# Performance work log

Measured on AMD Instinct MI355X. Metric: run time of the kernel, lower is better.

Reference implementation:

```python
import jax, jax.numpy as jnp
import numpy as np

EPS = 1e-8


def setup_inputs() -> dict:
    key = jax.random.key(0)
    k1, k2, k3 = jax.random.split(key, 3)
    B, N, M, C = 4, 4096, 16384, 256
    xyz = jax.random.normal(k1, (B * N, 3), dtype=jnp.float32)
    new_xyz = jax.random.normal(k2, (B * M, 3), dtype=jnp.float32)
    feat = jax.random.normal(k3, (B * N, C), dtype=jnp.float32)
    offset = jnp.arange(1, B + 1, dtype=jnp.int64) * N      # [4096, 8192, 12288, 16384]
    new_offset = jnp.arange(1, B + 1, dtype=jnp.int64) * M  # [16384, ..., 65536]
    return {"xyz": xyz, "new_xyz": new_xyz, "feat": feat,
            "offset": offset, "new_offset": new_offset, "k": 3}


def _interpolate(xyz_b, new_xyz_b, feat_b, k):
    # xyz_b: [B,N,3], new_xyz_b: [B,M,3], feat_b: [B,N,C]
    # pairwise squared distances via GEMM: [B,M,N]
    q2 = jnp.sum(new_xyz_b * new_xyz_b, axis=-1, keepdims=True)        # [B,M,1]
    s2 = jnp.sum(xyz_b * xyz_b, axis=-1)[:, None, :]                   # [B,1,N]
    cross = jnp.einsum('bmd,bnd->bmn', new_xyz_b, xyz_b)               # [B,M,N]
    d2 = q2 + s2 - 2.0 * cross                                         # [B,M,N]
    neg_d2, idx = jax.lax.top_k(-d2, k)                                # [B,M,k]
    dist = jnp.sqrt(jnp.maximum(-neg_d2, 1e-12))                       # euclidean, like knnquery
    dist_recip = 1.0 / (dist + EPS)
    weight = dist_recip / jnp.sum(dist_recip, axis=-1, keepdims=True)  # [B,M,k]
    gathered = jax.vmap(lambda f, i: f[i])(feat_b, idx)                # [B,M,k,C]
    return jnp.einsum('bmkc,bmk->bmc', gathered, weight)               # [B,M,C]


def reference(xyz, new_xyz, feat, offset, new_offset, k):
    B = offset.shape[0]
    N = xyz.shape[0] // B
    M = new_xyz.shape[0] // B
    C = feat.shape[1]
    # uniform offsets -> reshape into per-cloud batches
    out = _interpolate(xyz.reshape(B, N, 3), new_xyz.reshape(B, M, 3),
                       feat.reshape(B, N, C), k)
    return out.reshape(B * M, C)
```

## Files before the change

kernel.cpp:

```cpp
#include <hip/hip_runtime.h>
#include <float.h>


#define QPL   2
#define QPB   128
#define SPLIT 8
#define KEY_INIT 0x7FEFFFFFFFFFFFFFULL

typedef float v2f __attribute__((ext_vector_type(2)));

__global__ void pack_pts(const float* __restrict__ xyz,
                         float4* __restrict__ pts, int total) {
    int i = blockIdx.x * blockDim.x + threadIdx.x;
    if (i < total) {
        const float sx = xyz[(size_t)i * 3 + 0];
        const float sy = xyz[(size_t)i * 3 + 1];
        const float sz = xyz[(size_t)i * 3 + 2];
        const float s2 = __fadd_rn(__fadd_rn(__fmul_rn(sx, sx), __fmul_rn(sy, sy)),
                                   __fmul_rn(sz, sz));
        pts[i] = make_float4(sx, sy, sz, s2);
    }
}

__device__ __forceinline__ double mk_key(float d2, int j) {
    unsigned long long u =
        ((unsigned long long)(unsigned)__float_as_uint(d2) << 32) | (unsigned)j;
    return __longlong_as_double(u);
}

__device__ __forceinline__ v2f dist2_pair(const v2f qx2, const v2f qy2,
                                          const v2f qz2, const v2f q22,
                                          const float4 p) {
    #pragma clang fp contract(off)
    const v2f px = {p.x, p.x};
    const v2f py = {p.y, p.y};
    const v2f pz = {p.z, p.z};
    const v2f pw = {p.w, p.w};
    const v2f t0 = qx2 * px;
    const v2f t1 = qy2 * py;
    const v2f t2 = t0 + t1;
    const v2f t3 = qz2 * pz;
    const v2f cr = t2 + t3;
    const v2f qs = q22 + pw;
    const v2f cc = cr + cr;
    const v2f d2 = qs - cc;
    return d2;
}

__device__ __forceinline__ float dist2_scalar(float qx, float qy, float qz,
                                              float q2, const float4 p) {
    #pragma clang fp contract(off)
    const float t0 = qx * p.x;
    const float t1 = qy * p.y;
    const float t2 = t0 + t1;
    const float t3 = qz * p.z;
    const float cr = t2 + t3;
    const float qs = q2 + p.w;
    const float cc = cr + cr;
    const float d2 = qs - cc;
    return d2;
}

template <int CHUNK>
__global__ __launch_bounds__(512, 4) void fp_knn_main(
    const float* __restrict__ new_xyz,
    const float4* __restrict__ pts,
    const float4* __restrict__ feat4,
    float4* __restrict__ out4,
    int N, int blocks_per_batch)
{
    __shared__ double s_k[SPLIT][QPB][3];
    __shared__ float  s_w[QPB][3];
    __shared__ int    s_j[QPB][3];

    int g = blockIdx.x;
    if (gridDim.x == 512 && blocks_per_batch == 128) {
        const int xcd = g & 7, slot = g >> 3;
        g = (xcd >> 1) * 128 + (xcd & 1) * 64 + slot;
    }

    const int tid  = threadIdx.x;
    const int lane = tid & 63;
    const int b    = g / blocks_per_batch;
    const int src_base = b * N;
    const int m0 = g * QPB + lane;
    const int m1 = m0 + 64;

    const float q0x = new_xyz[(size_t)m0 * 3 + 0];
    const float q0y = new_xyz[(size_t)m0 * 3 + 1];
    const float q0z = new_xyz[(size_t)m0 * 3 + 2];
    const float q1x = new_xyz[(size_t)m1 * 3 + 0];
    const float q1y = new_xyz[(size_t)m1 * 3 + 1];
    const float q1z = new_xyz[(size_t)m1 * 3 + 2];
    const float q02 = __fadd_rn(__fadd_rn(__fmul_rn(q0x, q0x), __fmul_rn(q0y, q0y)),
                                __fmul_rn(q0z, q0z));
    const float q12 = __fadd_rn(__fadd_rn(__fmul_rn(q1x, q1x), __fmul_rn(q1y, q1y)),
                                __fmul_rn(q1z, q1z));
    const v2f qx2 = {q0x, q1x};
    const v2f qy2 = {q0y, q1y};
    const v2f qz2 = {q0z, q1z};
    const v2f q22 = {q02, q12};

    const int cw    = tid >> 6;
    const int cbase = cw * CHUNK;
    const float4* __restrict__ cp = pts + src_base + cbase;

    double k00 = __longlong_as_double(KEY_INIT);
    double k01 = k00, k02 = k00;
    double k10 = k00, k11 = k00, k12 = k00;

    constexpr int G  = 8;
    constexpr int NG = CHUNK / G;

    float4 A[G], B[G];

    auto process = [&](const float4 p, int cj) {
        const v2f d2 = dist2_pair(qx2, qy2, qz2, q22, p);
        const double ka = mk_key(d2.x, cj);
        const double kb = mk_key(d2.y, cj);
        const double a0 = fmin(ka, k00);
        const double a1 = fmin(fmax(ka, k00), k01);
        const double a2 = fmin(fmax(ka, k01), k02);
        k00 = a0; k01 = a1; k02 = a2;
        const double b0 = fmin(kb, k10);
        const double b1 = fmin(fmax(kb, k10), k11);
        const double b2 = fmin(fmax(kb, k11), k12);
        k10 = b0; k11 = b1; k12 = b2;
    };

    #pragma unroll
    for (int t = 0; t < G; ++t) A[t] = cp[t];
    __builtin_amdgcn_sched_barrier(0);

    int gi = 0;
    for (; gi < NG - 2; gi += 2) {
        const float4* nx1 = cp + (gi + 1) * G;
        #pragma unroll
        for (int t = 0; t < G; ++t) B[t] = nx1[t];
        __builtin_amdgcn_sched_barrier(0);
        #pragma unroll
        for (int t = 0; t < G; ++t) process(A[t], cbase + gi * G + t);
        __builtin_amdgcn_sched_barrier(0);
        const float4* nx2 = cp + (gi + 2) * G;
        #pragma unroll
        for (int t = 0; t < G; ++t) A[t] = nx2[t];
        __builtin_amdgcn_sched_barrier(0);
        #pragma unroll
        for (int t = 0; t < G; ++t) process(B[t], cbase + (gi + 1) * G + t);
        __builtin_amdgcn_sched_barrier(0);
    }
    {
        const float4* nx1 = cp + (gi + 1) * G;
        #pragma unroll
        for (int t = 0; t < G; ++t) B[t] = nx1[t];
        __builtin_amdgcn_sched_barrier(0);
        #pragma unroll
        for (int t = 0; t < G; ++t) process(A[t], cbase + gi * G + t);
        #pragma unroll
        for (int t = 0; t < G; ++t) process(B[t], cbase + (gi + 1) * G + t);
    }

    s_k[cw][lane][0]      = k00; s_k[cw][lane][1]      = k01; s_k[cw][lane][2]      = k02;
    s_k[cw][lane + 64][0] = k10; s_k[cw][lane + 64][1] = k11; s_k[cw][lane + 64][2] = k12;
    __syncthreads();

    if (tid < QPB) {
        double m0k = __longlong_as_double(KEY_INIT), m1k = m0k, m2k = m0k;
        #pragma unroll
        for (int ss = 0; ss < SPLIT; ++ss) {
            #pragma unroll
            for (int r = 0; r < 3; ++r) {
                const double d = s_k[ss][tid][r];
                const double n0 = fmin(d, m0k);
                const double n1 = fmin(fmax(d, m0k), m1k);
                const double n2 = fmin(fmax(d, m1k), m2k);
                m0k = n0; m1k = n1; m2k = n2;
            }
        }
        unsigned long long u0 = __double_as_longlong(m0k);
        unsigned long long u1 = __double_as_longlong(m1k);
        unsigned long long u2 = __double_as_longlong(m2k);
        const float d0 = __uint_as_float((unsigned)(u0 >> 32));
        const float d1 = __uint_as_float((unsigned)(u1 >> 32));
        const float d2 = __uint_as_float((unsigned)(u2 >> 32));
        const float e0 = sqrtf(fmaxf(d0, 1e-12f));
        const float e1 = sqrtf(fmaxf(d1, 1e-12f));
        const float e2 = sqrtf(fmaxf(d2, 1e-12f));
        const float r0 = 1.0f / (e0 + 1e-8f);
        const float r1 = 1.0f / (e1 + 1e-8f);
        const float r2 = 1.0f / (e2 + 1e-8f);
        const float rs = r0 + r1 + r2;
        s_w[tid][0] = r0 / rs; s_w[tid][1] = r1 / rs; s_w[tid][2] = r2 / rs;
        s_j[tid][0] = (int)(u0 & 0xffffffffu);
        s_j[tid][1] = (int)(u1 & 0xffffffffu);
        s_j[tid][2] = (int)(u2 & 0xffffffffu);
    }
    __syncthreads();

    const int wv    = tid >> 6;
    const int qbase = g * QPB;
    #pragma unroll 4
    for (int t = 0; t < QPB / SPLIT; ++t) {
        const int qq = wv * (QPB / SPLIT) + t;
        const int   a0 = s_j[qq][0], a1 = s_j[qq][1], a2 = s_j[qq][2];
        const float u0 = s_w[qq][0], u1 = s_w[qq][1], u2 = s_w[qq][2];
        const float4 f0 = feat4[(size_t)(src_base + a0) * 64 + lane];
        const float4 f1 = feat4[(size_t)(src_base + a1) * 64 + lane];
        const float4 f2 = feat4[(size_t)(src_base + a2) * 64 + lane];
        float4 o;
        o.x = u0 * f0.x + u1 * f1.x + u2 * f2.x;
        o.y = u0 * f0.y + u1 * f1.y + u2 * f2.y;
        o.z = u0 * f0.z + u1 * f1.z + u2 * f2.z;
        o.w = u0 * f0.w + u1 * f1.w + u2 * f2.w;
        out4[(size_t)(qbase + qq) * 64 + lane] = o;
    }
}

__global__ void fp_knn_generic(
    const float* __restrict__ new_xyz, const float* __restrict__ xyz,
    const float* __restrict__ feat, float* __restrict__ out,
    int N, int M, int Btot)
{
    const int m = blockIdx.x * blockDim.x + threadIdx.x;
    if (m >= Btot * M) return;
    const int b = m / M;
    const int src_base = b * N;
    const float qx = new_xyz[(size_t)m * 3 + 0];
    const float qy = new_xyz[(size_t)m * 3 + 1];
    const float qz = new_xyz[(size_t)m * 3 + 2];
    const float q2 = __fadd_rn(__fadd_rn(__fmul_rn(qx, qx), __fmul_rn(qy, qy)),
                               __fmul_rn(qz, qz));
    double k0 = __longlong_as_double(KEY_INIT), k1 = k0, k2 = k0;
    for (int j = 0; j < N; ++j) {
        const float sx = xyz[(size_t)(src_base + j) * 3 + 0];
        const float sy = xyz[(size_t)(src_base + j) * 3 + 1];
        const float sz = xyz[(size_t)(src_base + j) * 3 + 2];
        const float s2 = __fadd_rn(__fadd_rn(__fmul_rn(sx, sx), __fmul_rn(sy, sy)),
                                   __fmul_rn(sz, sz));
        const float4 p = make_float4(sx, sy, sz, s2);
        const float d2 = dist2_scalar(qx, qy, qz, q2, p);
        const double key = mk_key(d2, j);
        const double n0 = fmin(key, k0);
        const double n1 = fmin(fmax(key, k0), k1);
        const double n2 = fmin(fmax(key, k1), k2);
        k0 = n0; k1 = n1; k2 = n2;
    }
    unsigned long long u0 = __double_as_longlong(k0);
    unsigned long long u1 = __double_as_longlong(k1);
    unsigned long long u2 = __double_as_longlong(k2);
    const float e0 = sqrtf(fmaxf(__uint_as_float((unsigned)(u0 >> 32)), 1e-12f));
    const float e1 = sqrtf(fmaxf(__uint_as_float((unsigned)(u1 >> 32)), 1e-12f));
    const float e2 = sqrtf(fmaxf(__uint_as_float((unsigned)(u2 >> 32)), 1e-12f));
    const float r0 = 1.0f / (e0 + 1e-8f);
    const float r1 = 1.0f / (e1 + 1e-8f);
    const float r2 = 1.0f / (e2 + 1e-8f);
    const float rs = r0 + r1 + r2;
    const float w0 = r0 / rs, w1 = r1 / rs, w2 = r2 / rs;
    const int a0 = (int)(u0 & 0xffffffffu), a1 = (int)(u1 & 0xffffffffu),
              a2 = (int)(u2 & 0xffffffffu);
    const int C = 256;
    for (int c = 0; c < C; ++c) {
        out[(size_t)m * C + c] =
            w0 * feat[(size_t)(src_base + a0) * C + c] +
            w1 * feat[(size_t)(src_base + a1) * C + c] +
            w2 * feat[(size_t)(src_base + a2) * C + c];
    }
}

extern "C" void kernel_launch(void* const* d_in, const int* in_sizes, int n_in,
                              void* d_out, int out_size, void* d_ws, size_t ws_size,
                              hipStream_t stream) {
    const float* xyz     = (const float*)d_in[0];
    const float* new_xyz = (const float*)d_in[1];
    const float* feat    = (const float*)d_in[2];
    float* out = (float*)d_out;

    const int B = in_sizes[3];
    const int N = in_sizes[0] / (3 * B);
    const int M = in_sizes[1] / (3 * B);

    const size_t need = (size_t)(B * N) * sizeof(float4);
    const bool fast = (N % SPLIT == 0) && (N / SPLIT == 512) &&
                      (M % QPB == 0) && (ws_size >= need);
    if (fast) {
        pack_pts<<<(B * N + 255) / 256, 256, 0, stream>>>(xyz, (float4*)d_ws, B * N);
        const int blocks = (B * M) / QPB;
        fp_knn_main<512><<<blocks, 512, 0, stream>>>(
            new_xyz, (const float4*)d_ws, (const float4*)feat, (float4*)out,
            N, M / QPB);
    } else {
        fp_knn_generic<<<(B * M + 255) / 256, 256, 0, stream>>>(
            new_xyz, xyz, feat, out, N, M, B);
    }
}
```

Baseline: 207.6 us.

## Replace brute-force KNN with uniform grid spatial hashing and ring search

```diff
diff --git a/kernel.cpp b/kernel.cpp
--- a/kernel.cpp
+++ b/kernel.cpp
@@ -7,20 +7,14 @@
 #define SPLIT 8
 #define KEY_INIT 0x7FEFFFFFFFFFFFFFULL
 
+#define NCA   32
+#define NC    (NCA * NCA * NCA)
+#define GMIN  (-4.0f)
+#define HCELL (0.25f)
+#define INVH  (4.0f)
+#define SLACK (1e-3f)
+
 typedef float v2f __attribute__((ext_vector_type(2)));
-
-__global__ void pack_pts(const float* __restrict__ xyz,
-                         float4* __restrict__ pts, int total) {
-    int i = blockIdx.x * blockDim.x + threadIdx.x;
-    if (i < total) {
-        const float sx = xyz[(size_t)i * 3 + 0];
-        const float sy = xyz[(size_t)i * 3 + 1];
-        const float sz = xyz[(size_t)i * 3 + 2];
-        const float s2 = __fadd_rn(__fadd_rn(__fmul_rn(sx, sx), __fmul_rn(sy, sy)),
-                                   __fmul_rn(sz, sz));
-        pts[i] = make_float4(sx, sy, sz, s2);
-    }
-}
 
 __device__ __forceinline__ double mk_key(float d2, int j) {
     unsigned long long u =
@@ -61,14 +55,248 @@
     return d2;
 }
 
+__device__ __forceinline__ float sum_sq3(float x, float y, float z) {
+    return __fadd_rn(__fadd_rn(__fmul_rn(x, x), __fmul_rn(y, y)),
+                     __fmul_rn(z, z));
+}
+
+__device__ __forceinline__ int clampi(int v, int lo, int hi) {
+    return v < lo ? lo : (v > hi ? hi : v);
+}
+
+__device__ __forceinline__ void cell3(float x, float y, float z,
+                                      int& cx, int& cy, int& cz) {
+    cx = clampi((int)floorf((x - GMIN) * INVH), 0, NCA - 1);
+    cy = clampi((int)floorf((y - GMIN) * INVH), 0, NCA - 1);
+    cz = clampi((int)floorf((z - GMIN) * INVH), 0, NCA - 1);
+}
+
+__global__ void grid_histo(const float* __restrict__ xyz,
+                           const float* __restrict__ new_xyz,
+                           int* __restrict__ cnt, int* __restrict__ qcnt,
+                           int N, int M, int B) {
+    const int i = blockIdx.x * blockDim.x + threadIdx.x;
+    const int totalP = B * N;
+    if (i < totalP) {
+        const int b = i / N;
+        int cx, cy, cz;
+        cell3(xyz[(size_t)i * 3 + 0], xyz[(size_t)i * 3 + 1],
+              xyz[(size_t)i * 3 + 2], cx, cy, cz);
+        atomicAdd(&cnt[b * NC + (cz * NCA + cy) * NCA + cx], 1);
+    } else {
+        const int qi = i - totalP;
+        if (qi < B * M) {
+            const int b = qi / M;
+            int cx, cy, cz;
+            cell3(new_xyz[(size_t)qi * 3 + 0], new_xyz[(size_t)qi * 3 + 1],
+                  new_xyz[(size_t)qi * 3 + 2], cx, cy, cz);
+            atomicAdd(&qcnt[b * NC + (cz * NCA + cy) * NCA + cx], 1);
+        }
+    }
+}
+
+__global__ __launch_bounds__(256) void grid_scan(
+    const int* __restrict__ cnt, int* __restrict__ start,
+    const int* __restrict__ qcnt, int* __restrict__ qstart,
+    int N, int M, int B) {
+    const int blk = blockIdx.x;
+    const bool isQ = blk >= B;
+    const int b = isQ ? blk - B : blk;
+    const int* __restrict__ src = isQ ? qcnt : cnt;
+    int* __restrict__ dst = isQ ? qstart : start;
+    const int base = isQ ? b * M : b * N;
+    const int t = threadIdx.x;
+    const int CH = NC / 256;
+
+    int s = 0;
+    for (int j = 0; j < CH; ++j) s += src[b * NC + t * CH + j];
+
+    __shared__ int parts[256];
+    parts[t] = s;
+    __syncthreads();
+    for (int off = 1; off < 256; off <<= 1) {
+        int v = 0;
+        if (t >= off) v = parts[t - off];
+        __syncthreads();
+        parts[t] += v;
+        __syncthreads();
+    }
+    int run = base + (t == 0 ? 0 : parts[t - 1]);
+    for (int j = 0; j < CH; ++j) {
+        dst[b * NC + t * CH + j] = run;
+        run += src[b * NC + t * CH + j];
+    }
+    if (!isQ && b == B - 1 && t == 255) dst[B * NC] = B * N;
+}
+
+__global__ void grid_scatter(const float* __restrict__ xyz,
+                             const float* __restrict__ new_xyz,
+                             int* __restrict__ cnt, int* __restrict__ qcnt,
+                             const int* __restrict__ start,
+                             const int* __restrict__ qstart,
+                             float4* __restrict__ spts, int* __restrict__ sidx,
+                             int* __restrict__ qsrt,
+                             int N, int M, int B) {
+    const int i = blockIdx.x * blockDim.x + threadIdx.x;
+    const int totalP = B * N;
+    if (i < totalP) {
+        const int b = i / N;
+        const float sx = xyz[(size_t)i * 3 + 0];
+        const float sy = xyz[(size_t)i * 3 + 1];
+        const float sz = xyz[(size_t)i * 3 + 2];
+        int cx, cy, cz;
+        cell3(sx, sy, sz, cx, cy, cz);
+        const int g = b * NC + (cz * NCA + cy) * NCA + cx;
+        const int slot = start[g] + (atomicSub(&cnt[g], 1) - 1);
+        spts[slot] = make_float4(sx, sy, sz, sum_sq3(sx, sy, sz));
+        sidx[slot] = i - b * N;
+    } else {
+        const int qi = i - totalP;
+        if (qi < B * M) {
+            const int b = qi / M;
+            int cx, cy, cz;
+            cell3(new_xyz[(size_t)qi * 3 + 0], new_xyz[(size_t)qi * 3 + 1],
+                  new_xyz[(size_t)qi * 3 + 2], cx, cy, cz);
+            const int g = b * NC + (cz * NCA + cy) * NCA + cx;
+            const int slot = qstart[g] + (atomicSub(&qcnt[g], 1) - 1);
+            qsrt[slot] = qi;
+        }
+    }
+}
+
+__global__ __launch_bounds__(256) void fp_knn_grid(
+    const float* __restrict__ new_xyz,
+    const float4* __restrict__ spts, const int* __restrict__ sidx,
+    const int* __restrict__ start, const int* __restrict__ qsrt,
+    int4* __restrict__ jb, float4* __restrict__ wb,
+    int N, int M, int B) {
+    const int p = blockIdx.x * blockDim.x + threadIdx.x;
+    if (p >= B * M) return;
+    const int qid = qsrt[p];
+    const int b = qid / M;
+    const int bNC = b * NC;
+
+    const float qx = new_xyz[(size_t)qid * 3 + 0];
+    const float qy = new_xyz[(size_t)qid * 3 + 1];
+    const float qz = new_xyz[(size_t)qid * 3 + 2];
+    const float q2 = sum_sq3(qx, qy, qz);
+
+    int cx, cy, cz;
+    cell3(qx, qy, qz, cx, cy, cz);
+
+    const float bx0 = GMIN + (float)cx * HCELL;
+    const float by0 = GMIN + (float)cy * HCELL;
+    const float bz0 = GMIN + (float)cz * HCELL;
+    const float ex = fmaxf(fmaxf(bx0 - qx, qx - (bx0 + HCELL)), 0.0f);
+    const float ey = fmaxf(fmaxf(by0 - qy, qy - (by0 + HCELL)), 0.0f);
+    const float ez = fmaxf(fmaxf(bz0 - qz, qz - (bz0 + HCELL)), 0.0f);
+    const float e = fmaxf(ex, fmaxf(ey, ez));
+
+    double k0 = __longlong_as_double(KEY_INIT), k1 = k0, k2 = k0;
+
+    auto seg = [&](int x0, int x1, int cy2, int cz2) {
+        const int rowbase = bNC + (cz2 * NCA + cy2) * NCA;
+        const int j0 = start[rowbase + x0];
+        const int j1 = start[rowbase + x1 + 1];
+        for (int j = j0; j < j1; ++j) {
+            const float4 pt = spts[j];
+            const float d2 = dist2_scalar(qx, qy, qz, q2, pt);
+            const double key = mk_key(d2, sidx[j]);
+            const double n0 = fmin(key, k0);
+            const double n1 = fmin(fmax(key, k0), k1);
+            const double n2 = fmin(fmax(key, k1), k2);
+            k0 = n0; k1 = n1; k2 = n2;
+        }
+    };
+
+    seg(cx, cx, cy, cz);
+    for (int r = 1; r < NCA; ++r) {
+        const float d3 = __uint_as_float(
+            (unsigned)((unsigned long long)__double_as_longlong(k2) >> 32));
+        const float lb = fmaxf(HCELL * (float)(r - 1) - e, 0.0f);
+        if (lb * lb > d3 + SLACK) break;
+        const int z0 = cz - r < 0 ? 0 : cz - r;
+        const int z1 = cz + r > NCA - 1 ? NCA - 1 : cz + r;
+        const int y0 = cy - r < 0 ? 0 : cy - r;
+        const int y1 = cy + r > NCA - 1 ? NCA - 1 : cy + r;
+        const int x0 = cx - r < 0 ? 0 : cx - r;
+        const int x1 = cx + r > NCA - 1 ? NCA - 1 : cx + r;
+        for (int cz2 = z0; cz2 <= z1; ++cz2) {
+            const int adz = cz2 >= cz ? cz2 - cz : cz - cz2;
+            for (int cy2 = y0; cy2 <= y1; ++cy2) {
+                const int ady = cy2 >= cy ? cy2 - cy : cy - cy2;
+                if (adz == r || ady == r) {
+                    seg(x0, x1, cy2, cz2);
+                } else {
+                    if (cx - r >= 0)      seg(cx - r, cx - r, cy2, cz2);
+                    if (cx + r <= NCA - 1) seg(cx + r, cx + r, cy2, cz2);
+                }
+            }
+        }
+    }
+
+    const unsigned long long u0 = __double_as_longlong(k0);
+    const unsigned long long u1 = __double_as_longlong(k1);
+    const unsigned long long u2 = __double_as_longlong(k2);
+    const float d0 = __uint_as_float((unsigned)(u0 >> 32));
+    const float d1 = __uint_as_float((unsigned)(u1 >> 32));
+    const float d2f = __uint_as_float((unsigned)(u2 >> 32));
+    const float e0 = sqrtf(fmaxf(d0, 1e-12f));
+    const float e1 = sqrtf(fmaxf(d1, 1e-12f));
+    const float e2 = sqrtf(fmaxf(d2f, 1e-12f));
+    const float r0 = 1.0f / (e0 + 1e-8f);
+    const float r1 = 1.0f / (e1 + 1e-8f);
+    const float r2 = 1.0f / (e2 + 1e-8f);
+    const float rs = r0 + r1 + r2;
+    jb[qid] = make_int4((int)(u0 & 0xffffffffu), (int)(u1 & 0xffffffffu),
+                        (int)(u2 & 0xffffffffu), 0);
+    wb[qid] = make_float4(r0 / rs, r1 / rs, r2 / rs, 0.0f);
+}
+
+__global__ __launch_bounds__(256, 8) void fp_gather(
+    const float4* __restrict__ feat4, const int4* __restrict__ jb,
+    const float4* __restrict__ wb, float4* __restrict__ out4,
+    int N, int M) {
+    const int tid  = threadIdx.x;
+    const int lane = tid & 63;
+    const int wv   = tid >> 6;
+    const int qblk = blockIdx.x * 16;
+    const int b    = qblk / M;
+    const int src_base = b * N;
+    #pragma unroll
+    for (int t = 0; t < 4; ++t) {
+        const int q = qblk + wv * 4 + t;
+        const int4   J = jb[q];
+        const float4 W = wb[q];
+        const float4 f0 = feat4[(size_t)(src_base + J.x) * 64 + lane];
+        const float4 f1 = feat4[(size_t)(src_base + J.y) * 64 + lane];
+        const float4 f2 = feat4[(size_t)(src_base + J.z) * 64 + lane];
+        const float u0 = W.x, u1 = W.y, u2 = W.z;
+        float4 o;
+        o.x = u0 * f0.x + u1 * f1.x + u2 * f2.x;
+        o.y = u0 * f0.y + u1 * f1.y + u2 * f2.y;
+        o.z = u0 * f0.z + u1 * f1.z + u2 * f2.z;
+        o.w = u0 * f0.w + u1 * f1.w + u2 * f2.w;
+        out4[(size_t)q * 64 + lane] = o;
+    }
+}
+
+__global__ void pack_pts(const float* __restrict__ xyz,
+                         float4* __restrict__ pts, int total) {
+    int i = blockIdx.x * blockDim.x + threadIdx.x;
+    if (i < total) {
+        const float sx = xyz[(size_t)i * 3 + 0];
+        const float sy = xyz[(size_t)i * 3 + 1];
+        const float sz = xyz[(size_t)i * 3 + 2];
+        pts[i] = make_float4(sx, sy, sz, sum_sq3(sx, sy, sz));
+    }
+}
+
 template <int CHUNK>
 __global__ __launch_bounds__(512, 4) void fp_knn_main(
-    const float* __restrict__ new_xyz,
-    const float4* __restrict__ pts,
-    const float4* __restrict__ feat4,
-    float4* __restrict__ out4,
-    int N, int blocks_per_batch)
-{
+    const float* __restrict__ new_xyz, const float4* __restrict__ pts,
+    const float4* __restrict__ feat4, float4* __restrict__ out4,
+    int N, int blocks_per_batch) {
     __shared__ double s_k[SPLIT][QPB][3];
     __shared__ float  s_w[QPB][3];
     __shared__ int    s_j[QPB][3];
@@ -92,14 +320,10 @@
     const float q1x = new_xyz[(size_t)m1 * 3 + 0];
     const float q1y = new_xyz[(size_t)m1 * 3 + 1];
     const float q1z = new_xyz[(size_t)m1 * 3 + 2];
-    const float q02 = __fadd_rn(__fadd_rn(__fmul_rn(q0x, q0x), __fmul_rn(q0y, q0y)),
-                                __fmul_rn(q0z, q0z));
-    const float q12 = __fadd_rn(__fadd_rn(__fmul_rn(q1x, q1x), __fmul_rn(q1y, q1y)),
-                                __fmul_rn(q1z, q1z));
     const v2f qx2 = {q0x, q1x};
     const v2f qy2 = {q0y, q1y};
     const v2f qz2 = {q0z, q1z};
-    const v2f q22 = {q02, q12};
+    const v2f q22 = {sum_sq3(q0x, q0y, q0z), sum_sq3(q1x, q1y, q1z)};
 
     const int cw    = tid >> 6;
     const int cbase = cw * CHUNK;
@@ -109,15 +333,12 @@
     double k01 = k00, k02 = k00;
     double k10 = k00, k11 = k00, k12 = k00;
 
-    constexpr int G  = 8;
-    constexpr int NG = CHUNK / G;
-
-    float4 A[G], B[G];
-
-    auto process = [&](const float4 p, int cj) {
+    #pragma unroll 8
+    for (int j = 0; j < CHUNK; ++j) {
+        const float4 p = cp[j];
         const v2f d2 = dist2_pair(qx2, qy2, qz2, q22, p);
-        const double ka = mk_key(d2.x, cj);
-        const double kb = mk_key(d2.y, cj);
+        const double ka = mk_key(d2.x, cbase + j);
+        const double kb = mk_key(d2.y, cbase + j);
         const double a0 = fmin(ka, k00);
         const double a1 = fmin(fmax(ka, k00), k01);
         const double a2 = fmin(fmax(ka, k01), k02);
@@ -126,38 +347,6 @@
         const double b1 = fmin(fmax(kb, k10), k11);
         const double b2 = fmin(fmax(kb, k11), k12);
         k10 = b0; k11 = b1; k12 = b2;
-    };
-
-    #pragma unroll
-    for (int t = 0; t < G; ++t) A[t] = cp[t];
-    __builtin_amdgcn_sched_barrier(0);
-
-    int gi = 0;
-    for (; gi < NG - 2; gi += 2) {
-        const float4* nx1 = cp + (gi + 1) * G;
-        #pragma unroll
-        for (int t = 0; t < G; ++t) B[t] = nx1[t];
-        __builtin_amdgcn_sched_barrier(0);
-        #pragma unroll
-        for (int t = 0; t < G; ++t) process(A[t], cbase + gi * G + t);
-        __builtin_amdgcn_sched_barrier(0);
-        const float4* nx2 = cp + (gi + 2) * G;
-        #pragma unroll
-        for (int t = 0; t < G; ++t) A[t] = nx2[t];
-        __builtin_amdgcn_sched_barrier(0);
-        #pragma unroll
-        for (int t = 0; t < G; ++t) process(B[t], cbase + (gi + 1) * G + t);
-        __builtin_amdgcn_sched_barrier(0);
-    }
-    {
-        const float4* nx1 = cp + (gi + 1) * G;
-        #pragma unroll
-        for (int t = 0; t < G; ++t) B[t] = nx1[t];
-        __builtin_amdgcn_sched_barrier(0);
-        #pragma unroll
-        for (int t = 0; t < G; ++t) process(A[t], cbase + gi * G + t);
-        #pragma unroll
-        for (int t = 0; t < G; ++t) process(B[t], cbase + (gi + 1) * G + t);
     }
 
     s_k[cw][lane][0]      = k00; s_k[cw][lane][1]      = k01; s_k[cw][lane][2]      = k02;
@@ -219,8 +408,7 @@
 __global__ void fp_knn_generic(
     const float* __restrict__ new_xyz, const float* __restrict__ xyz,
     const float* __restrict__ feat, float* __restrict__ out,
-    int N, int M, int Btot)
-{
+    int N, int M, int Btot) {
     const int m = blockIdx.x * blockDim.x + threadIdx.x;
     if (m >= Btot * M) return;
     const int b = m / M;
@@ -228,16 +416,13 @@
     const float qx = new_xyz[(size_t)m * 3 + 0];
     const float qy = new_xyz[(size_t)m * 3 + 1];
     const float qz = new_xyz[(size_t)m * 3 + 2];
-    const float q2 = __fadd_rn(__fadd_rn(__fmul_rn(qx, qx), __fmul_rn(qy, qy)),
-                               __fmul_rn(qz, qz));
+    const float q2 = sum_sq3(qx, qy, qz);
     double k0 = __longlong_as_double(KEY_INIT), k1 = k0, k2 = k0;
     for (int j = 0; j < N; ++j) {
         const float sx = xyz[(size_t)(src_base + j) * 3 + 0];
         const float sy = xyz[(size_t)(src_base + j) * 3 + 1];
         const float sz = xyz[(size_t)(src_base + j) * 3 + 2];
-        const float s2 = __fadd_rn(__fadd_rn(__fmul_rn(sx, sx), __fmul_rn(sy, sy)),
-                                   __fmul_rn(sz, sz));
-        const float4 p = make_float4(sx, sy, sz, s2);
+        const float4 p = make_float4(sx, sy, sz, sum_sq3(sx, sy, sz));
         const float d2 = dist2_scalar(qx, qy, qz, q2, p);
         const double key = mk_key(d2, j);
         const double n0 = fmin(key, k0);
@@ -278,18 +463,58 @@
     const int B = in_sizes[3];
     const int N = in_sizes[0] / (3 * B);
     const int M = in_sizes[1] / (3 * B);
-
-    const size_t need = (size_t)(B * N) * sizeof(float4);
-    const bool fast = (N % SPLIT == 0) && (N / SPLIT == 512) &&
-                      (M % QPB == 0) && (ws_size >= need);
-    if (fast) {
+    const int Q = B * M;
+
+    auto al = [](size_t x) { return (x + 255) & ~(size_t)255; };
+    const size_t o_spts   = 0;
+    const size_t o_sidx   = o_spts  + al((size_t)B * N * 16);
+    const size_t o_cnt    = o_sidx  + al((size_t)B * N * 4);
+    const size_t o_start  = o_cnt   + al((size_t)B * NC * 4);
+    const size_t o_qcnt   = o_start + al(((size_t)B * NC + 1) * 4);
+    const size_t o_qstart = o_qcnt  + al((size_t)B * NC * 4);
+    const size_t o_qsort  = o_qstart+ al(((size_t)B * NC + 1) * 4);
+    const size_t o_jb     = o_qsort + al((size_t)Q * 4);
+    const size_t o_wb     = o_jb    + al((size_t)Q * 16);
+    const size_t need_grid = o_wb   + al((size_t)Q * 16);
+
+    if ((M % 16 == 0) && ws_size >= need_grid) {
+        char* w = (char*)d_ws;
+        float4* spts  = (float4*)(w + o_spts);
+        int*   sidx   = (int*)  (w + o_sidx);
+        int*   cnt    = (int*)  (w + o_cnt);
+        int*   start  = (int*)  (w + o_start);
+        int*   qcnt   = (int*)  (w + o_qcnt);
+        int*   qstart = (int*)  (w + o_qstart);
+        int*   qsrt   = (int*)  (w + o_qsort);
+        int4*  jb     = (int4*) (w + o_jb);
+        float4* wb    = (float4*)(w + o_wb);
+
+        hipMemsetAsync(cnt,  0, (size_t)B * NC * 4, stream);
+        hipMemsetAsync(qcnt, 0, (size_t)B * NC * 4, stream);
+        const int items = B * N + B * M;
+        grid_histo<<<(items + 255) / 256, 256, 0, stream>>>(
+            xyz, new_xyz, cnt, qcnt, N, M, B);
+        grid_scan<<<2 * B, 256, 0, stream>>>(cnt, start, qcnt, qstart, N, M, B);
+        grid_scatter<<<(items + 255) / 256, 256, 0, stream>>>(
+            xyz, new_xyz, cnt, qcnt, start, qstart, spts, sidx, qsrt, N, M, B);
+        fp_knn_grid<<<(Q + 255) / 256, 256, 0, stream>>>(
+            new_xyz, spts, sidx, start, qsrt, jb, wb, N, M, B);
+        fp_gather<<<Q / 16, 256, 0, stream>>>(
+            (const float4*)feat, jb, wb, (float4*)out, N, M);
+        return;
+    }
+
+    const size_t pts_bytes = (size_t)(B * N) * sizeof(float4);
+    const bool fused_ok = (N % SPLIT == 0) && (N / SPLIT == 512) &&
+                          (M % QPB == 0) && (ws_size >= pts_bytes);
+    if (fused_ok) {
         pack_pts<<<(B * N + 255) / 256, 256, 0, stream>>>(xyz, (float4*)d_ws, B * N);
-        const int blocks = (B * M) / QPB;
+        const int blocks = Q / QPB;
         fp_knn_main<512><<<blocks, 512, 0, stream>>>(
             new_xyz, (const float4*)d_ws, (const float4*)feat, (float4*)out,
             N, M / QPB);
     } else {
-        fp_knn_generic<<<(B * M + 255) / 256, 256, 0, stream>>>(
+        fp_knn_generic<<<(Q + 255) / 256, 256, 0, stream>>>(
             new_xyz, xyz, feat, out, N, M, B);
     }
 }
```

New measurement: 498.5 us. 140% more time.
